# Performance work log

Measured on AMD Instinct MI355X. Metric: run time of the kernel, lower is better.

## Reference

```python
import jax, jax.numpy as jnp
import numpy as np

EPS = 1e-5


def setup_inputs() -> dict:
    key = jax.random.key(0)
    ks = jax.random.split(key, 10)
    B, C, H, W = 4, 256, 64, 64
    x = jax.random.normal(ks[0], (B, C, H, W), dtype=jnp.float32)
    s = 1.0 / np.sqrt(C)
    inp = {
        "x": x,
        "gn_w": jnp.ones((C,), jnp.float32),
        "gn_b": jnp.zeros((C,), jnp.float32),
        "wq": jax.random.normal(ks[1], (C, C), jnp.float32) * s,
        "bq": jnp.zeros((C,), jnp.float32),
        "wk": jax.random.normal(ks[2], (C, C), jnp.float32) * s,
        "bk": jnp.zeros((C,), jnp.float32),
        "wv": jax.random.normal(ks[3], (C, C), jnp.float32) * s,
        "bv": jnp.zeros((C,), jnp.float32),
        "wo": jax.random.normal(ks[4], (C, C), jnp.float32) * s,
        "bo": jnp.zeros((C,), jnp.float32),
    }
    return inp


def _forward(x, gn_w, gn_b, wq, bq, wk, bk, wv, bv, wo, bo):
    B, C, H, W = x.shape
    G = C // 2  # num_groups = channels // 2 -> 2 channels per group
    # GroupNorm
    xg = x.reshape(B, G, C // G, H, W)
    mu = jnp.mean(xg, axis=(2, 3, 4), keepdims=True)
    var = jnp.var(xg, axis=(2, 3, 4), keepdims=True)
    hn = ((xg - mu) * jax.lax.rsqrt(var + EPS)).reshape(B, C, H, W)
    hn = hn * gn_w[None, :, None, None] + gn_b[None, :, None, None]
    # tokens: (B, N, C), N = H*W
    h = hn.transpose(0, 2, 3, 1).reshape(B, H * W, C)
    q = h @ wq.T + bq
    k = h @ wk.T + bk
    v = h @ wv.T + bv
    # full NxN attention, scaled by C^-0.5 (as in original)
    scores = jnp.einsum("bnc,bmc->bnm", q, k) * (C ** -0.5)
    attn = jax.nn.softmax(scores, axis=-1)
    h2 = jnp.einsum("bnm,bmc->bnc", attn, v)  # (B, N, C)
    # faithful replication of the original's layout-scrambling reshape:
    # (B,N,C) -> (B,H,W,C) -> permute (B,C,H,W) -> reshape (B,HW,C)
    h2 = h2.reshape(B, H, W, C).transpose(0, 3, 1, 2).reshape(B, H * W, C)
    out = (h2 @ wo.T + bo).reshape(B, C, H, W)
    return x + out


def reference(x, gn_w, gn_b, wq, bq, wk, bk, wv, bv, wo, bo):
    return _forward(x, gn_w, gn_b, wq, bq, wk, bk, wv, bv, wo, bo)
```

## Files before the change

### kernel.cpp

```cpp
#include <hip/hip_runtime.h>

typedef unsigned short u16;
typedef unsigned int   u32;
typedef __attribute__((ext_vector_type(8)))  short short8;
typedef __attribute__((ext_vector_type(4)))  float f32x4;
typedef __attribute__((ext_vector_type(16))) float f32x16;

#define DI __device__ __forceinline__

DI u16 f2bf(float f){
  u32 u = __builtin_bit_cast(u32, f);
  u += 0x7fffu + ((u >> 16) & 1u);
  return (u16)(u >> 16);
}

DI void gl_lds16(const void* g, void* l){
  __builtin_amdgcn_global_load_lds((const __attribute__((address_space(1))) void*)g,
                                   (__attribute__((address_space(3))) void*)l, 16, 0, 0);
}

DI f32x4 mfma16(short8 a, short8 b, f32x4 c){
  return __builtin_amdgcn_mfma_f32_16x16x32_bf16(a, b, c, 0, 0, 0);
}
DI f32x16 mfma32(short8 a, short8 b, f32x16 c){
  return __builtin_amdgcn_mfma_f32_32x32x16_bf16(a, b, c, 0, 0, 0);
}
DI f32x16 z16(){
  f32x16 v;
  #pragma unroll
  for (int i=0;i<16;i++) v[i]=0.f;
  return v;
}

union U8 { u32 u[4]; short8 s; };

#define OFF_WBF   0u
#define OFF_STATS (512u<<10)
#define OFF_HTOK  (1u<<20)
#define OFF_Q     ((1u<<20) + (8u<<20))
#define OFF_K     ((1u<<20) + (16u<<20))
#define OFF_VT    ((1u<<20) + (24u<<20))
#define OFF_H2T   OFF_Q
#define OFF_PART  ((1u<<20) + (32u<<20))
#define OFF_ML    ((1u<<20) + (96u<<20))

__global__ void k_prep(const float* w0, const float* w1, const float* w2, const float* w3, u16* wbf){
  const float* src = (blockIdx.y==0)?w0:(blockIdx.y==1)?w1:(blockIdx.y==2)?w2:w3;
  u16* d = wbf + blockIdx.y*65536;
  int i = (blockIdx.x*256 + threadIdx.x)*4;
  float4 v = *(const float4*)(src + i);
  u32 lo = (u32)f2bf(v.x) | ((u32)f2bf(v.y)<<16);
  u32 hi = (u32)f2bf(v.z) | ((u32)f2bf(v.w)<<16);
  *(uint2*)(d + i) = make_uint2(lo, hi);
}

__global__ void k_gnstats(const float* x, float2* stats){
  int bg = blockIdx.x;
  const float* p = x + (size_t)bg*8192;
  float s = 0.f, ss = 0.f;
  #pragma unroll
  for (int i=0;i<8;i++){
    float4 v = *(const float4*)(p + threadIdx.x*4 + i*1024);
    s  += v.x+v.y+v.z+v.w;
    ss += v.x*v.x + v.y*v.y + v.z*v.z + v.w*v.w;
  }
  #pragma unroll
  for (int off=1; off<64; off<<=1){ s += __shfl_xor(s, off, 64); ss += __shfl_xor(ss, off, 64); }
  __shared__ float as[4], aq[4];
  int w = threadIdx.x>>6;
  if ((threadIdx.x&63)==0){ as[w]=s; aq[w]=ss; }
  __syncthreads();
  if (threadIdx.x==0){
    s = as[0]+as[1]+as[2]+as[3]; ss = aq[0]+aq[1]+aq[2]+aq[3];
    float mu = s * (1.f/8192.f);
    float var = ss * (1.f/8192.f) - mu*mu;
    stats[bg] = make_float2(mu, rsqrtf(var + 1e-5f));
  }
}

__global__ void k_gnapply(const float* x, const float* gw, const float* gb,
                          const float2* stats, u16* htok){
  __shared__ u16 tile[64*256];
  int b = blockIdx.y, n0 = blockIdx.x*64, t = threadIdx.x;
  const float* xb = x + (size_t)b*1048576;
  #pragma unroll
  for (int p=0;p<4;p++){
    int c = p*64 + (t>>2);
    float2 st = stats[b*128 + (c>>1)];
    float scl = st.y * gw[c];
    float off = gb[c] - st.x*scl;
    const float* src = xb + (size_t)c*4096 + n0 + (t&3)*16;
    #pragma unroll
    for (int u2=0;u2<4;u2++){
      float4 v = *(const float4*)(src + u2*4);
      float vv[4] = {v.x,v.y,v.z,v.w};
      #pragma unroll
      for (int j=0;j<4;j++){
        int n = (t&3)*16 + u2*4 + j;
        int addr = n*512 + ((c*2) ^ ((n&7)<<4));
        *(u16*)((char*)tile + addr) = f2bf(vv[j]*scl + off);
      }
    }
  }
  __syncthreads();
  int n = t>>2, seg = t&3;
  char* dst = (char*)(htok + ((size_t)(b*4096 + n0 + n)*256 + seg*64));
  #pragma unroll
  for (int i=0;i<8;i++){
    int boff = n*512 + (((seg*128) + i*16) ^ ((n&7)<<4));
    *(uint4*)(dst + i*16) = *(const uint4*)((const char*)tile + boff);
  }
}

DI void stage_w(const u16* Wg, int dk, u16* dst, int w, int l){
  const char* Wb = (const char*)Wg;
  #pragma unroll
  for (int i=0;i<8;i++){
    int cout = w*64 + i*8 + (l>>3);
    gl_lds16(Wb + cout*512 + dk*128 + (((l&7)*16) ^ ((cout&7)<<4)), dst + w*4096 + i*512);
  }
}

DI void gemm_tile(const u16* Ag, const u16* Wg, int row0, int t,
                  u16* lds_a, u16* w0, u16* w1, f32x4 acc[4][4]){
  const int w = t>>6, l = t&63, lo = l&15, hi = l>>4;
  const char* Ab = (const char*)Ag + (size_t)row0*512;
  #pragma unroll
  for (int i=0;i<8;i++){
    int row = w*16 + i*2 + (l>>5);
    gl_lds16(Ab + row*512 + (((l&31)*16) ^ ((row&7)<<4)), lds_a + w*4096 + i*512);
  }
  stage_w(Wg, 0, w0, w, l);
  __syncthreads();
  u16* wb[2] = {w0, w1};
  #pragma unroll
  for (int dk=0; dk<4; dk++){
    if (dk<3) stage_w(Wg, dk+1, wb[(dk+1)&1], w, l);
    const char* wc = (const char*)wb[dk&1];
    #pragma unroll
    for (int s=0;s<2;s++){
      short8 af[4], bf[4];
      #pragma unroll
      for (int rg=0;rg<4;rg++){
        int row = rg*16 + lo;
        af[rg] = *(const short8*)((const char*)lds_a + row*512 + ((dk*128 + s*64 + hi*16) ^ ((row&7)<<4)));
      }
      #pragma unroll
      for (int cf=0;cf<4;cf++){
        int col = w*64 + cf*16 + lo;
        bf[cf] = *(const short8*)(wc + col*128 + ((s*64 + hi*16) ^ ((col&7)<<4)));
      }
      #pragma unroll
      for (int rg=0;rg<4;rg++)
        #pragma unroll
        for (int cf=0;cf<4;cf++)
          acc[rg][cf] = mfma16(af[rg], bf[cf], acc[rg][cf]);
    }
    __syncthreads();
  }
}

__global__ __launch_bounds__(256,1) void k_qkv(const u16* htok, const u16* wbf,
    const float* bq, const float* bk, const float* bv,
    u16* qo, u16* ko, u16* vt){
  __shared__ u16 lds_a[64*256];
  __shared__ u16 lds_w[2][256*64];
  const int t = threadIdx.x, mode = blockIdx.y, row0 = blockIdx.x*64;
  const u16* W = wbf + mode*65536;
  const float* bias = (mode==0)?bq:((mode==1)?bk:bv);
  f32x4 acc[4][4];
  #pragma unroll
  for (int i=0;i<4;i++)
    #pragma unroll
    for (int j=0;j<4;j++) acc[i][j] = (f32x4){0.f,0.f,0.f,0.f};
  gemm_tile(htok, W, row0, t, lds_a, lds_w[0], lds_w[1], acc);
  const int w = t>>6, l = t&63, lo = l&15, hi = l>>4;
  if (mode < 2){
    float scl = (mode==0)? 0.09016844f : 1.0f;
    u16* dst = (mode==0)? qo : ko;
    #pragma unroll
    for (int rg=0;rg<4;rg++)
      #pragma unroll
      for (int cf=0;cf<4;cf++){
        int col = w*64 + cf*16 + lo;
        float bs = bias[col];
        #pragma unroll
        for (int r=0;r<4;r++){
          int grow = row0 + rg*16 + hi*4 + r;
          dst[(size_t)grow*256 + col] = f2bf((acc[rg][cf][r] + bs)*scl);
        }
      }
  } else {
    __syncthreads();
    #pragma unroll
    for (int rg=0;rg<4;rg++)
      #pragma unroll
      for (int cf=0;cf<4;cf++){
        int col = w*64 + cf*16 + lo;
        float bs = bias[col];
        ushort4 pk;
        pk.x = f2bf(acc[rg][cf][0]+bs); pk.y = f2bf(acc[rg][cf][1]+bs);
        pk.z = f2bf(acc[rg][cf][2]+bs); pk.w = f2bf(acc[rg][cf][3]+bs);
        int rl = rg*16 + hi*4;
        int addr = col*128 + ((rl*2) ^ ((col&7)<<4));
        *(ushort4*)((char*)lds_a + addr) = pk;
      }
    __syncthreads();
    int b = row0 >> 12, nb = row0 & 4095;
    #pragma unroll
    for (int p=0;p<8;p++){
      int c = p*32 + (t>>3), i = t&7;
      uint4 vd = *(const uint4*)((const char*)lds_a + c*128 + ((i*16) ^ ((c&7)<<4)));
      *(uint4*)((char*)vt + ((size_t)(b*256 + c)*4096 + nb)*2 + i*16) = vd;
    }
  }
}

__global__ __launch_bounds__(256,1) void k_out(const u16* h2t, const u16* wo,
    const float* bo, const float* x, float* out){
  __shared__ u16 lds_a[64*256];
  __shared__ u16 lds_w[2][256*64];
  const int t = threadIdx.x, row0 = blockIdx.x*64;
  f32x4 acc[4][4];
  #pragma unroll
  for (int i=0;i<4;i++)
    #pragma unroll
    for (int j=0;j<4;j++) acc[i][j] = (f32x4){0.f,0.f,0.f,0.f};
  gemm_tile(h2t, wo, row0, t, lds_a, lds_w[0], lds_w[1], acc);
  const int w = t>>6, l = t&63, lo = l&15, hi = l>>4;
  #pragma unroll
  for (int rg=0;rg<4;rg++)
    #pragma unroll
    for (int cf=0;cf<4;cf++){
      int col = w*64 + cf*16 + lo;
      float bs = bo[col];
      #pragma unroll
      for (int r=0;r<4;r++){
        size_t flat = (size_t)(row0 + rg*16 + hi*4 + r)*256 + col;
        out[flat] = x[flat] + acc[rg][cf][r] + bs;
      }
    }
}

__global__ __launch_bounds__(512,2) void k_attn(const u16* q, const u16* k,
                                                const u16* vt, u16* part, float2* ml){
  __shared__ char smem[131072];
  const int t = threadIdx.x, w = t>>6, l = t&63;
  const int lq = l&31, h = l>>5;
  const int bid = blockIdx.x;
  const int x = bid&7, idx = bid>>3;
  const int combo = x*2 + (idx&1);
  const int b = combo>>2, ks = combo&3, qt = idx>>1;

  const char* kg = (const char*)k  + ((size_t)b*4096 + (size_t)ks*1024)*512;
  const char* vg = (const char*)vt + (size_t)b*2097152 + (size_t)ks*2048;

  short8 qf[16];
  {
    const char* qrow = (const char*)q + ((size_t)b*4096 + qt*256 + w*32 + lq)*512;
    #pragma unroll
    for (int dk=0;dk<16;dk++) qf[dk] = *(const short8*)(qrow + dk*32 + h*16);
  }

  f32x16 O[8];
  #pragma unroll
  for (int ct=0;ct<8;ct++) O[ct] = z16();
  float m_run = -1e30f, l_run = 0.f;

  auto stage = [&](int ti, int buf){
    #pragma unroll
    for (int sub=0; sub<2; ++sub){
      char* kd = smem + buf*32768 + sub*16384;
      char* vd = smem + 65536 + buf*32768 + sub*16384;
      #pragma unroll
      for (int j=0;j<2;j++){
        int key = w*4 + j*2 + h;
        gl_lds16(kg + (size_t)(ti*64 + sub*32 + key)*512 + (((l&31)*16) ^ ((key&7)<<4)),
                 kd + (w*2+j)*1024);
      }
      #pragma unroll
      for (int j=0;j<2;j++){
        int c = w*32 + j*16 + (l>>2);
        gl_lds16(vg + (size_t)c*8192 + ti*128 + sub*64 + (((l&3)*16) ^ (((l>>3)&3)<<4)),
                 vd + (w*2+j)*1024);
      }
    }
  };

  stage(0, 0);
  __syncthreads();

  for (int tile=0; tile<16; ++tile){
    const int cur = tile&1;
    if (tile < 15) stage(tile+1, cur^1);
    #pragma unroll
    for (int sub=0; sub<2; ++sub){
      const char* kbuf = smem + cur*32768 + sub*16384;
      const char* vbuf = smem + 65536 + cur*32768 + sub*16384;

      f32x16 sa = z16(), sb = z16();
      __builtin_amdgcn_s_setprio(1);
      #pragma unroll
      for (int dk=0;dk<16;dk+=2){
        short8 ka = *(const short8*)(kbuf + (size_t)lq*512 + ((dk*32     + h*16) ^ ((lq&7)<<4)));
        short8 kc2= *(const short8*)(kbuf + (size_t)lq*512 + (((dk+1)*32 + h*16) ^ ((lq&7)<<4)));
        sa = mfma32(ka,  qf[dk],   sa);
        sb = mfma32(kc2, qf[dk+1], sb);
      }
      __builtin_amdgcn_s_setprio(0);
      float s[16];
      #pragma unroll
      for (int r=0;r<16;r++) s[r] = sa[r] + sb[r];

      float pmax = s[0];
      #pragma unroll
      for (int r=1;r<16;r++) pmax = fmaxf(pmax, s[r]);
      pmax = fmaxf(pmax, __shfl_xor(pmax, 32, 64));
      if (__any(pmax > m_run + 8.f)){
        float mn = fmaxf(m_run, pmax);
        float sclq = exp2f(m_run - mn);
        m_run = mn;
        l_run *= sclq;
        #pragma unroll
        for (int r=0;r<16;r++){
          float sr = __shfl(sclq, (r&3)+8*(r>>2)+4*h, 64);
          #pragma unroll
          for (int ct=0;ct<8;ct++) O[ct][r] *= sr;
        }
      }
      float p[16]; float ps = 0.f;
      #pragma unroll
      for (int r=0;r<16;r++){ p[r] = exp2f(s[r] - m_run); ps += p[r]; }
      l_run += ps + __shfl_xor(ps, 32, 64);
      u32 pk[8];
      #pragma unroll
      for (int j=0;j<8;j++){
        u32 u0 = __builtin_bit_cast(u32, p[2*j]);
        u32 u1 = __builtin_bit_cast(u32, p[2*j+1]);
        pk[j] = (u1 & 0xffff0000u) | (u0 >> 16);
      }

      #pragma unroll
      for (int kc=0;kc<2;kc++){
        u32 sA = h ? pk[4*kc]   : pk[4*kc+2];
        u32 sB = h ? pk[4*kc+1] : pk[4*kc+3];
        u32 xA = __shfl_xor(sA, 32, 64);
        u32 xB = __shfl_xor(sB, 32, 64);
        U8 pa;
        pa.u[0] = h ? xA : pk[4*kc];
        pa.u[1] = h ? xB : pk[4*kc+1];
        pa.u[2] = h ? pk[4*kc+2] : xA;
        pa.u[3] = h ? pk[4*kc+3] : xB;
        __builtin_amdgcn_s_setprio(1);
        #pragma unroll
        for (int ct=0;ct<8;ct++){
          short8 vb = *(const short8*)(vbuf + (size_t)(ct*32+lq)*64 + ((kc*32 + h*16) ^ (((lq>>1)&3)<<4)));
          O[ct] = mfma32(pa.s, vb, O[ct]);
        }
        __builtin_amdgcn_s_setprio(0);
      }
    }
    __syncthreads();
  }

  if (h == 0)
    ml[(size_t)combo*4096 + qt*256 + w*32 + lq] = make_float2(m_run, l_run);
  u16* otile = (u16*)smem;
  char* pbase = (char*)part + ((size_t)combo*4096 + (size_t)qt*256)*512;
  #pragma unroll
  for (int rd=0; rd<2; ++rd){
    __syncthreads();
    if ((w>>2) == rd){
      int wl = w&3;
      #pragma unroll
      for (int ct=0;ct<8;ct++)
        #pragma unroll
        for (int r=0;r<16;r++){
          int row = wl*32 + (r&3) + 8*(r>>2) + 4*h;
          otile[row*256 + ct*32 + lq] = f2bf(O[ct][r]);
        }
    }
    __syncthreads();
    const char* sb2 = (const char*)smem;
    char* gb2 = pbase + (size_t)rd*65536;
    #pragma unroll
    for (int j=0;j<8;j++)
      *(uint4*)(gb2 + t*16 + (size_t)j*8192) = *(const uint4*)(sb2 + t*16 + (size_t)j*8192);
  }
}

__global__ __launch_bounds__(256,2) void k_combine(const u16* part, const float2* ml, u16* h2t){
  __shared__ u16 tile[64*256];
  const int t = threadIdx.x, b = blockIdx.y, n0 = blockIdx.x*64;
  const int n = t>>2, cc = (t&3)*64;
  const int gn = n0 + n;
  float2 st[4]; float ms = -1e30f;
  #pragma unroll
  for (int ksi=0;ksi<4;ksi++){ st[ksi] = ml[(size_t)(b*4+ksi)*4096 + gn]; ms = fmaxf(ms, st[ksi].x); }
  float wn[4]; float denom = 0.f;
  #pragma unroll
  for (int ksi=0;ksi<4;ksi++){ wn[ksi] = exp2f(st[ksi].x - ms); denom += wn[ksi]*st[ksi].y; }
  float inv = 1.f/denom;
  #pragma unroll
  for (int ksi=0;ksi<4;ksi++) wn[ksi] *= inv;
  float acc[64];
  #pragma unroll
  for (int j=0;j<64;j++) acc[j] = 0.f;
  #pragma unroll
  for (int ksi=0;ksi<4;ksi++){
    const u16* src = part + ((size_t)(b*4+ksi)*4096 + gn)*256 + cc;
    float wv = wn[ksi];
    #pragma unroll
    for (int j8=0;j8<8;j8++){
      short8 v = *(const short8*)(src + j8*8);
      #pragma unroll
      for (int e=0;e<8;e++){
        u32 uu = ((u32)(u16)v[e])<<16;
        acc[j8*8+e] += wv * __builtin_bit_cast(float, uu);
      }
    }
  }
  char* tb = (char*)tile;
  #pragma unroll
  for (int j=0;j<32;j++){
    u32 pkv = ((u32)f2bf(acc[2*j+1])<<16) | f2bf(acc[2*j]);
    *(u32*)(tb + n*512 + ((cc*2 + j*4) ^ ((n&7)<<4))) = pkv;
  }
  __syncthreads();
  {
    const char* tbc = (const char*)tile;
    u32 outw[32];
    #pragma unroll
    for (int j=0;j<32;j++){
      u16 v0 = *(const u16*)(tbc + (2*j  )*512 + ((t*2) ^ (((2*j  )&7)<<4)));
      u16 v1 = *(const u16*)(tbc + (2*j+1)*512 + ((t*2) ^ (((2*j+1)&7)<<4)));
      outw[j] = ((u32)v1<<16) | v0;
    }
    char* dst = (char*)h2t + ((size_t)(b*256 + t)*4096 + n0)*2;
    #pragma unroll
    for (int j=0;j<8;j++){
      uint4 vv; vv.x = outw[4*j]; vv.y = outw[4*j+1]; vv.z = outw[4*j+2]; vv.w = outw[4*j+3];
      *(uint4*)(dst + j*16) = vv;
    }
  }
}

extern "C" void kernel_launch(void* const* d_in, const int* in_sizes, int n_in,
                              void* d_out, int out_size, void* d_ws, size_t ws_size,
                              hipStream_t stream) {
  const float* x    = (const float*)d_in[0];
  const float* gn_w = (const float*)d_in[1];
  const float* gn_b = (const float*)d_in[2];
  const float* wq   = (const float*)d_in[3];
  const float* bq   = (const float*)d_in[4];
  const float* wk   = (const float*)d_in[5];
  const float* bk   = (const float*)d_in[6];
  const float* wv   = (const float*)d_in[7];
  const float* bv   = (const float*)d_in[8];
  const float* wo   = (const float*)d_in[9];
  const float* bo   = (const float*)d_in[10];
  float* out = (float*)d_out;
  char* ws = (char*)d_ws;

  u16*    wbf   = (u16*)(ws + OFF_WBF);
  float2* stats = (float2*)(ws + OFF_STATS);
  u16*    htok  = (u16*)(ws + OFF_HTOK);
  u16*    qb    = (u16*)(ws + OFF_Q);
  u16*    kb    = (u16*)(ws + OFF_K);
  u16*    vt    = (u16*)(ws + OFF_VT);
  u16*    h2t   = (u16*)(ws + OFF_H2T);
  u16*    part  = (u16*)(ws + OFF_PART);
  float2* ml    = (float2*)(ws + OFF_ML);

  k_prep   <<<dim3(64,4), 256, 0, stream>>>(wq, wk, wv, wo, wbf);
  k_gnstats<<<512,        256, 0, stream>>>(x, stats);
  k_gnapply<<<dim3(64,4), 256, 0, stream>>>(x, gn_w, gn_b, stats, htok);
  k_qkv    <<<dim3(256,3),256, 0, stream>>>(htok, wbf, bq, bk, bv, qb, kb, vt);
  k_attn   <<<256,        512, 0, stream>>>(qb, kb, vt, part, ml);
  k_combine<<<dim3(64,4), 256, 0, stream>>>(part, ml, h2t);
  k_out    <<<256,        256, 0, stream>>>(h2t, wbf + 3*65536, bo, x, out);
}
```

Baseline: 192.8 us.

## Split attention head dim across wave pairs and software-pipeline QK^T with softmax

The attention kernel now gives each block 128 query rows instead of 256, doubling the grid. Each pair of waves shares the same 32 query rows, and each wave in the pair accumulates half of the 256 output channels, so the O accumulator shrinks from 8 to 4 tiles. K/V staging becomes a 4-slot ring of 32-key sub-tiles, and the next sub-tile's QK^T MFMAs are issued before the current softmax/PV step to overlap matrix and vector work. In exchange, both waves of a pair compute the same QK^T scores and softmax, which adds redundant MFMA and exp work per key.

```diff
diff --git a/kernel.cpp b/kernel.cpp
--- a/kernel.cpp
+++ b/kernel.cpp
@@ -247,6 +247,7 @@
   __shared__ char smem[131072];
   const int t = threadIdx.x, w = t>>6, l = t&63;
   const int lq = l&31, h = l>>5;
+  const int pair = w>>1, dh = w&1;
   const int bid = blockIdx.x;
   const int x = bid&7, idx = bid>>3;
   const int combo = x*2 + (idx&1);
@@ -257,132 +258,142 @@
 
   short8 qf[16];
   {
-    const char* qrow = (const char*)q + ((size_t)b*4096 + qt*256 + w*32 + lq)*512;
+    const char* qrow = (const char*)q + ((size_t)b*4096 + qt*128 + pair*32 + lq)*512;
     #pragma unroll
     for (int dk=0;dk<16;dk++) qf[dk] = *(const short8*)(qrow + dk*32 + h*16);
   }
 
-  f32x16 O[8];
-  #pragma unroll
-  for (int ct=0;ct<8;ct++) O[ct] = z16();
+  f32x16 O[4];
+  #pragma unroll
+  for (int ct=0;ct<4;ct++) O[ct] = z16();
   float m_run = -1e30f, l_run = 0.f;
 
-  auto stage = [&](int ti, int buf){
-    #pragma unroll
-    for (int sub=0; sub<2; ++sub){
-      char* kd = smem + buf*32768 + sub*16384;
-      char* vd = smem + 65536 + buf*32768 + sub*16384;
-      #pragma unroll
-      for (int j=0;j<2;j++){
-        int key = w*4 + j*2 + h;
-        gl_lds16(kg + (size_t)(ti*64 + sub*32 + key)*512 + (((l&31)*16) ^ ((key&7)<<4)),
-                 kd + (w*2+j)*1024);
-      }
-      #pragma unroll
-      for (int j=0;j<2;j++){
-        int c = w*32 + j*16 + (l>>2);
-        gl_lds16(vg + (size_t)c*8192 + ti*128 + sub*64 + (((l&3)*16) ^ (((l>>3)&3)<<4)),
-                 vd + (w*2+j)*1024);
-      }
+  auto stage = [&](int sub){
+    char* kd = smem + (sub&3)*16384;
+    char* vd = smem + 65536 + (sub&3)*16384;
+    #pragma unroll
+    for (int j=0;j<2;j++){
+      int key = w*4 + j*2 + h;
+      gl_lds16(kg + (size_t)(sub*32 + key)*512 + (((l&31)*16) ^ ((key&7)<<4)),
+               kd + (w*2+j)*1024);
+    }
+    #pragma unroll
+    for (int j=0;j<2;j++){
+      int c = w*32 + j*16 + (l>>2);
+      gl_lds16(vg + (size_t)c*8192 + sub*64 + (((l&3)*16) ^ (((l>>3)&3)<<4)),
+               vd + (w*2+j)*1024);
     }
   };
 
-  stage(0, 0);
-  __syncthreads();
-
-  for (int tile=0; tile<16; ++tile){
-    const int cur = tile&1;
-    if (tile < 15) stage(tile+1, cur^1);
-    #pragma unroll
-    for (int sub=0; sub<2; ++sub){
-      const char* kbuf = smem + cur*32768 + sub*16384;
-      const char* vbuf = smem + 65536 + cur*32768 + sub*16384;
-
-      f32x16 sa = z16(), sb = z16();
+  auto qkt = [&](int sub, f32x16& sa, f32x16& sb){
+    const char* kbuf = smem + (sub&3)*16384;
+    sa = z16(); sb = z16();
+    __builtin_amdgcn_s_setprio(1);
+    #pragma unroll
+    for (int dk=0;dk<16;dk+=2){
+      short8 ka = *(const short8*)(kbuf + (size_t)lq*512 + ((dk*32     + h*16) ^ ((lq&7)<<4)));
+      short8 kc2= *(const short8*)(kbuf + (size_t)lq*512 + (((dk+1)*32 + h*16) ^ ((lq&7)<<4)));
+      sa = mfma32(ka,  qf[dk],   sa);
+      sb = mfma32(kc2, qf[dk+1], sb);
+    }
+    __builtin_amdgcn_s_setprio(0);
+  };
+
+  auto smpv = [&](int sub, const f32x16& sa, const f32x16& sb){
+    const char* vbuf = smem + 65536 + (sub&3)*16384;
+    float s[16];
+    #pragma unroll
+    for (int r=0;r<16;r++) s[r] = sa[r] + sb[r];
+    float mx[8];
+    #pragma unroll
+    for (int j=0;j<8;j++) mx[j] = fmaxf(s[2*j], s[2*j+1]);
+    #pragma unroll
+    for (int j=0;j<4;j++) mx[j] = fmaxf(mx[j], mx[j+4]);
+    float pmax = fmaxf(fmaxf(mx[0],mx[2]), fmaxf(mx[1],mx[3]));
+    pmax = fmaxf(pmax, __shfl_xor(pmax, 32, 64));
+    if (__any(pmax > m_run + 8.f)){
+      float mn = fmaxf(m_run, pmax);
+      float sclq = exp2f(m_run - mn);
+      m_run = mn;
+      l_run *= sclq;
+      #pragma unroll
+      for (int r=0;r<16;r++){
+        float sr = __shfl(sclq, (r&3)+8*(r>>2)+4*h, 64);
+        #pragma unroll
+        for (int ct=0;ct<4;ct++) O[ct][r] *= sr;
+      }
+    }
+    u32 pk[8];
+    float ps0 = 0.f, ps1 = 0.f;
+    #pragma unroll
+    for (int j=0;j<8;j++){
+      float p0 = exp2f(s[2*j]   - m_run);
+      float p1 = exp2f(s[2*j+1] - m_run);
+      ps0 += p0; ps1 += p1;
+      u32 u0 = __builtin_bit_cast(u32, p0);
+      u32 u1 = __builtin_bit_cast(u32, p1);
+      pk[j] = (u1 & 0xffff0000u) | (u0 >> 16);
+    }
+    float ps = ps0 + ps1;
+    l_run += ps + __shfl_xor(ps, 32, 64);
+    #pragma unroll
+    for (int kc=0;kc<2;kc++){
+      u32 sA = h ? pk[4*kc]   : pk[4*kc+2];
+      u32 sB = h ? pk[4*kc+1] : pk[4*kc+3];
+      u32 xA = __shfl_xor(sA, 32, 64);
+      u32 xB = __shfl_xor(sB, 32, 64);
+      U8 pa;
+      pa.u[0] = h ? xA : pk[4*kc];
+      pa.u[1] = h ? xB : pk[4*kc+1];
+      pa.u[2] = h ? pk[4*kc+2] : xA;
+      pa.u[3] = h ? pk[4*kc+3] : xB;
       __builtin_amdgcn_s_setprio(1);
       #pragma unroll
-      for (int dk=0;dk<16;dk+=2){
-        short8 ka = *(const short8*)(kbuf + (size_t)lq*512 + ((dk*32     + h*16) ^ ((lq&7)<<4)));
-        short8 kc2= *(const short8*)(kbuf + (size_t)lq*512 + (((dk+1)*32 + h*16) ^ ((lq&7)<<4)));
-        sa = mfma32(ka,  qf[dk],   sa);
-        sb = mfma32(kc2, qf[dk+1], sb);
+      for (int ct=0;ct<4;ct++){
+        int c = dh*128 + ct*32 + lq;
+        short8 vb = *(const short8*)(vbuf + (size_t)c*64 + ((kc*32 + h*16) ^ (((lq>>1)&3)<<4)));
+        O[ct] = mfma32(pa.s, vb, O[ct]);
       }
       __builtin_amdgcn_s_setprio(0);
-      float s[16];
-      #pragma unroll
-      for (int r=0;r<16;r++) s[r] = sa[r] + sb[r];
-
-      float pmax = s[0];
-      #pragma unroll
-      for (int r=1;r<16;r++) pmax = fmaxf(pmax, s[r]);
-      pmax = fmaxf(pmax, __shfl_xor(pmax, 32, 64));
-      if (__any(pmax > m_run + 8.f)){
-        float mn = fmaxf(m_run, pmax);
-        float sclq = exp2f(m_run - mn);
-        m_run = mn;
-        l_run *= sclq;
-        #pragma unroll
-        for (int r=0;r<16;r++){
-          float sr = __shfl(sclq, (r&3)+8*(r>>2)+4*h, 64);
-          #pragma unroll
-          for (int ct=0;ct<8;ct++) O[ct][r] *= sr;
-        }
-      }
-      float p[16]; float ps = 0.f;
-      #pragma unroll
-      for (int r=0;r<16;r++){ p[r] = exp2f(s[r] - m_run); ps += p[r]; }
-      l_run += ps + __shfl_xor(ps, 32, 64);
-      u32 pk[8];
-      #pragma unroll
-      for (int j=0;j<8;j++){
-        u32 u0 = __builtin_bit_cast(u32, p[2*j]);
-        u32 u1 = __builtin_bit_cast(u32, p[2*j+1]);
-        pk[j] = (u1 & 0xffff0000u) | (u0 >> 16);
-      }
-
-      #pragma unroll
-      for (int kc=0;kc<2;kc++){
-        u32 sA = h ? pk[4*kc]   : pk[4*kc+2];
-        u32 sB = h ? pk[4*kc+1] : pk[4*kc+3];
-        u32 xA = __shfl_xor(sA, 32, 64);
-        u32 xB = __shfl_xor(sB, 32, 64);
-        U8 pa;
-        pa.u[0] = h ? xA : pk[4*kc];
-        pa.u[1] = h ? xB : pk[4*kc+1];
-        pa.u[2] = h ? pk[4*kc+2] : xA;
-        pa.u[3] = h ? pk[4*kc+3] : xB;
-        __builtin_amdgcn_s_setprio(1);
-        #pragma unroll
-        for (int ct=0;ct<8;ct++){
-          short8 vb = *(const short8*)(vbuf + (size_t)(ct*32+lq)*64 + ((kc*32 + h*16) ^ (((lq>>1)&3)<<4)));
-          O[ct] = mfma32(pa.s, vb, O[ct]);
-        }
-        __builtin_amdgcn_s_setprio(0);
-      }
-    }
+    }
+  };
+
+  f32x16 saA, sbA, saB, sbB;
+  stage(0); stage(1);
+  __syncthreads();
+  qkt(0, saA, sbA);
+  for (int it=0; it<30; it+=2){
+    qkt(it+1, saB, sbB);
+    stage(it+2);
+    smpv(it, saA, sbA);
     __syncthreads();
-  }
-
-  if (h == 0)
-    ml[(size_t)combo*4096 + qt*256 + w*32 + lq] = make_float2(m_run, l_run);
+    qkt(it+2, saA, sbA);
+    stage(it+3);
+    smpv(it+1, saB, sbB);
+    __syncthreads();
+  }
+  qkt(31, saB, sbB);
+  smpv(30, saA, sbA);
+  __syncthreads();
+  smpv(31, saB, sbB);
+
+  if (h == 0 && dh == 0)
+    ml[(size_t)combo*4096 + qt*128 + pair*32 + lq] = make_float2(m_run, l_run);
+
+  __syncthreads();
   u16* otile = (u16*)smem;
-  char* pbase = (char*)part + ((size_t)combo*4096 + (size_t)qt*256)*512;
-  #pragma unroll
-  for (int rd=0; rd<2; ++rd){
-    __syncthreads();
-    if ((w>>2) == rd){
-      int wl = w&3;
-      #pragma unroll
-      for (int ct=0;ct<8;ct++)
-        #pragma unroll
-        for (int r=0;r<16;r++){
-          int row = wl*32 + (r&3) + 8*(r>>2) + 4*h;
-          otile[row*256 + ct*32 + lq] = f2bf(O[ct][r]);
-        }
-    }
-    __syncthreads();
+  #pragma unroll
+  for (int ct=0;ct<4;ct++)
+    #pragma unroll
+    for (int r=0;r<16;r++){
+      int row = pair*32 + (r&3) + 8*(r>>2) + 4*h;
+      int col = dh*128 + ct*32 + lq;
+      otile[row*256 + col] = f2bf(O[ct][r]);
+    }
+  __syncthreads();
+  {
     const char* sb2 = (const char*)smem;
-    char* gb2 = pbase + (size_t)rd*65536;
+    char* gb2 = (char*)part + ((size_t)combo*4096 + (size_t)qt*128)*512;
     #pragma unroll
     for (int j=0;j<8;j++)
       *(uint4*)(gb2 + t*16 + (size_t)j*8192) = *(const uint4*)(sb2 + t*16 + (size_t)j*8192);
@@ -476,7 +487,7 @@
   k_gnstats<<<512,        256, 0, stream>>>(x, stats);
   k_gnapply<<<dim3(64,4), 256, 0, stream>>>(x, gn_w, gn_b, stats, htok);
   k_qkv    <<<dim3(256,3),256, 0, stream>>>(htok, wbf, bq, bk, bv, qb, kb, vt);
-  k_attn   <<<256,        512, 0, stream>>>(qb, kb, vt, part, ml);
+  k_attn   <<<512,        512, 0, stream>>>(qb, kb, vt, part, ml);
   k_combine<<<dim3(64,4), 256, 0, stream>>>(part, ml, h2t);
   k_out    <<<256,        256, 0, stream>>>(h2t, wbf + 3*65536, bo, x, out);
 }
```

After: 208.7 us. 1.08x slower.
